# Performance work log

Measured on AMD Instinct MI355X. Metric: run time of the kernel, lower is better.

## Reference

```python
import jax, jax.numpy as jnp
import numpy as np

ALPHA = 0.2        # LeakyReLU negative slope (config['alpha'])
NEG_INF = -9e15    # mask value from the original code


def setup_inputs() -> dict:
    key = jax.random.key(0)
    k1, k2, k3, k4 = jax.random.split(key, 4)
    N, Fin, Fout = 8192, 512, 256
    inp = jax.random.normal(k1, (N, Fin), dtype=jnp.float32)
    adj = jax.random.randint(k2, (N, N), 0, 2, dtype=jnp.int32)
    # xavier_uniform with gain=1.414
    limW = 1.414 * np.sqrt(6.0 / (Fin + Fout))
    W = jax.random.uniform(k3, (Fin, Fout), dtype=jnp.float32, minval=-limW, maxval=limW)
    lima = 1.414 * np.sqrt(6.0 / (2 * Fout + 1))
    a = jax.random.uniform(k4, (2 * Fout, 1), dtype=jnp.float32, minval=-lima, maxval=lima)
    return {"input": inp, "adj": adj, "W": W, "a": a}


def reference(input, adj, W, a):
    # h: [N, F]
    h = input @ W
    Fout = W.shape[1]
    # The original builds a_input[i, j] = concat(h_i, h_j) and dots with a.
    # Equivalently: e_ij = leakyrelu(h_i . a[:F] + h_j . a[F:]), computed
    # without the O(N^2 * 2F) intermediate.
    s1 = h @ a[:Fout, 0]   # [N] contribution from node i
    s2 = h @ a[Fout:, 0]   # [N] contribution from node j
    e = s1[:, None] + s2[None, :]                     # [N, N]
    e = jnp.where(e > 0, e, ALPHA * e)                # LeakyReLU
    scores = jnp.where(adj > 0, e, NEG_INF)
    attention = jax.nn.softmax(scores, axis=1)        # row-wise softmax
    # dropout is identity in inference mode (training=False)
    h_prime = attention @ h                           # [N, F]
    return jax.nn.elu(h_prime)                        # concat=True path
```

## Files before the change

### kernel.cpp

```cpp
#include <hip/hip_runtime.h>
#include <stdint.h>
#include <stddef.h>


#define N_NODES 8192
#define FIN     512
#define FOUT    256
#define LRALPHA 0.2f
#define MI_SHIFT 16.0f

typedef float f32x4 __attribute__((ext_vector_type(4)));
typedef short s16x8 __attribute__((ext_vector_type(8)));
typedef unsigned short u16x4 __attribute__((ext_vector_type(4)));
typedef int   i32x4 __attribute__((ext_vector_type(4)));

__device__ __forceinline__ short f2bf_rne(float f) {
  uint32_t u = __builtin_bit_cast(uint32_t, f);
  u += 0x7fffu + ((u >> 16) & 1u);
  return (short)(u >> 16);
}
__device__ __forceinline__ short f2bf_fast(float f) {
  uint32_t u = __builtin_bit_cast(uint32_t, f);
  return (short)((u + 0x8000u) >> 16);
}
__device__ __forceinline__ float bf2f(short s) {
  uint32_t u = ((uint32_t)(uint16_t)s) << 16;
  return __builtin_bit_cast(float, u);
}

__global__ __launch_bounds__(256) void k_prep(const float* __restrict__ W,
                                              uint16_t* __restrict__ WThi,
                                              uint16_t* __restrict__ WTlo) {
  const int idx = blockIdx.x * 256 + threadIdx.x;
  const int n = idx >> 9;
  const int k = idx & 511;
  float v = W[k * FOUT + n];
  short h = f2bf_rne(v);
  WThi[idx] = (uint16_t)h;
  WTlo[idx] = (uint16_t)f2bf_rne(v - bf2f(h));
}

__global__ __launch_bounds__(256) void k_gemm_fused(const float* __restrict__ X,
                                                    const uint16_t* __restrict__ WThi,
                                                    const uint16_t* __restrict__ WTlo,
                                                    const float* __restrict__ a,
                                                    uint16_t* __restrict__ HTf,
                                                    float* __restrict__ s1g,
                                                    float* __restrict__ s2g) {
  __shared__ float ls1[16], ls2[16];
  __shared__ uint16_t tile[FOUT * 16];
  const int lane = threadIdx.x & 63;
  const int w    = threadIdx.x >> 6;
  const int m    = lane & 15;
  const int quad = lane >> 4;
  const int i0   = blockIdx.x * 16;
  const int colg = w * 64;

  f32x4 acc[4];
#pragma unroll
  for (int cb = 0; cb < 4; ++cb) { f32x4 z = {0.f,0.f,0.f,0.f}; acc[cb] = z; }

  for (int kt = 0; kt < FIN / 32; ++kt) {
    const int k0 = kt * 32 + quad * 8;
    const float* ap = X + (size_t)(i0 + m) * FIN + k0;
    f32x4 a0 = *(const f32x4*)ap;
    f32x4 a1 = *(const f32x4*)(ap + 4);
    s16x8 ahi, alo;
#pragma unroll
    for (int e = 0; e < 4; ++e) {
      short h0 = f2bf_rne(a0[e]); ahi[e] = h0; alo[e] = f2bf_rne(a0[e] - bf2f(h0));
      short h1 = f2bf_rne(a1[e]); ahi[4+e] = h1; alo[4+e] = f2bf_rne(a1[e] - bf2f(h1));
    }
#pragma unroll
    for (int cb = 0; cb < 4; ++cb) {
      const int n = colg + cb * 16 + m;
      s16x8 bhi = *(const s16x8*)(WThi + (size_t)n * FIN + k0);
      s16x8 blo = *(const s16x8*)(WTlo + (size_t)n * FIN + k0);
      acc[cb] = __builtin_amdgcn_mfma_f32_16x16x32_bf16(ahi, bhi, acc[cb], 0, 0, 0);
      acc[cb] = __builtin_amdgcn_mfma_f32_16x16x32_bf16(ahi, blo, acc[cb], 0, 0, 0);
      acc[cb] = __builtin_amdgcn_mfma_f32_16x16x32_bf16(alo, bhi, acc[cb], 0, 0, 0);
    }
  }

  float p1[4] = {0.f,0.f,0.f,0.f}, p2[4] = {0.f,0.f,0.f,0.f};
#pragma unroll
  for (int cb = 0; cb < 4; ++cb) {
    const int n = colg + cb * 16 + m;
    const float a1c = a[n];
    const float a2c = a[FOUT + n];
#pragma unroll
    for (int reg = 0; reg < 4; ++reg) {
      p1[reg] += acc[cb][reg] * a1c;
      p2[reg] += acc[cb][reg] * a2c;
    }
  }
#pragma unroll
  for (int off = 1; off <= 8; off <<= 1)
#pragma unroll
    for (int reg = 0; reg < 4; ++reg) {
      p1[reg] += __shfl_xor(p1[reg], off);
      p2[reg] += __shfl_xor(p2[reg], off);
    }
  if (threadIdx.x < 16) { ls1[threadIdx.x] = 0.f; ls2[threadIdx.x] = 0.f; }
  __syncthreads();
  if (m == 0) {
#pragma unroll
    for (int reg = 0; reg < 4; ++reg) {
      atomicAdd(&ls1[quad * 4 + reg], p1[reg]);
      atomicAdd(&ls2[quad * 4 + reg], p2[reg]);
    }
  }
#pragma unroll
  for (int cb = 0; cb < 4; ++cb) {
    const int col = colg + cb * 16 + m;
    u16x4 pk;
#pragma unroll
    for (int reg = 0; reg < 4; ++reg) pk[reg] = (uint16_t)f2bf_rne(acc[cb][reg]);
    *(u16x4*)(tile + col * 16 + quad * 4) = pk;
  }
  __syncthreads();
  const int t = threadIdx.x;
  if (t < 16) { s1g[i0 + t] = ls1[t]; s2g[i0 + t] = ls2[t]; }
  const int jt = i0 >> 5;
  const int qh = (i0 >> 4) & 1;
  const int c  = t >> 4;
  const int mm = t & 15;
#pragma unroll
  for (int qq = 0; qq < 2; ++qq) {
    uint4 v = *(const uint4*)(tile + (c * 16 + mm) * 16 + qq * 8);
    *(uint4*)(HTf + ((((size_t)jt * 16 + c) * 64) + (qh * 2 + qq) * 16 + mm) * 8) = v;
  }
}

__global__ __launch_bounds__(512, 8) void k_attn(const int* __restrict__ adj,
                                                 const uint16_t* __restrict__ HTf,
                                                 const float* __restrict__ s1,
                                                 const float* __restrict__ s2,
                                                 float* __restrict__ pout,
                                                 float* __restrict__ pden,
                                                 int split) {
  __shared__ uint16_t Pl[2][4096];
  __shared__ float ldsden[256];

  const int tid  = threadIdx.x;
  const int lane = tid & 63;
  const int w    = tid >> 6;
  const int m    = lane & 15;
  const int q    = lane >> 4;
  const int i0   = blockIdx.x * 32;
  const int sp   = blockIdx.y;
  const int jrange = N_NODES / split;
  const int jbeg   = sp * jrange;
  const int nphase = jrange / 128;
  const int rtp  = q >> 1;
  const int jq   = (q & 1) * 8;
  const int prow = i0 + rtp * 16 + m;

  const float s1r = s1[prow];
  float mi = s1r + MI_SHIFT; mi = mi > 0.f ? mi : LRALPHA * mi;

  f32x4 acc[2][2];
#pragma unroll
  for (int rt = 0; rt < 2; ++rt)
#pragma unroll
    for (int cb = 0; cb < 2; ++cb) { f32x4 z = {0.f,0.f,0.f,0.f}; acc[rt][cb] = z; }
  float den = 0.f;

  const int* arow = adj + (size_t)prow * N_NODES + jbeg + w * 16 + jq;
  const float* s2w = s2 + jbeg + w * 16 + jq;
  const int  pwoff = ((w * 2 + (q & 1)) * 32 + rtp * 16 + m) * 8;
  const uint16_t* hbase = HTf + ((size_t)(jbeg >> 5) * 16 + w * 2) * 64 * 8 + lane * 8;

  i32x4 A0 = *(const i32x4*)arow;
  i32x4 A1 = *(const i32x4*)(arow + 4);

#pragma unroll 1
  for (int p = 0; p < nphase; ++p) {
    const int poff = ((p + 1 < nphase) ? (p + 1) : 0) * 128;
    i32x4 nA0 = *(const i32x4*)(arow + poff);
    i32x4 nA1 = *(const i32x4*)(arow + poff + 4);
    f32x4 sv0 = *(const f32x4*)(s2w + p * 128);
    f32x4 sv1 = *(const f32x4*)(s2w + p * 128 + 4);
    s16x8 ap;
#pragma unroll
    for (int e = 0; e < 4; ++e) {
      float x = s1r + sv0[e];
      float t = x > 0.f ? x : LRALPHA * x;
      float pv = __expf(t - mi);
      pv = (A0[e] != 0) ? pv : 0.f;
      den += pv;
      ap[e] = f2bf_fast(pv);
    }
#pragma unroll
    for (int e = 0; e < 4; ++e) {
      float x = s1r + sv1[e];
      float t = x > 0.f ? x : LRALPHA * x;
      float pv = __expf(t - mi);
      pv = (A1[e] != 0) ? pv : 0.f;
      den += pv;
      ap[4 + e] = f2bf_fast(pv);
    }
    uint16_t* Pw = Pl[p & 1];
    *(s16x8*)(Pw + pwoff) = ap;
    A0 = nA0; A1 = nA1;
    __syncthreads();
    const uint16_t* hp = hbase + ((size_t)p * 4) * (16 * 64 * 8);
#pragma unroll
    for (int js = 0; js < 4; ++js) {
      s16x8 b0 = *(const s16x8*)(hp + (size_t)js * (16 * 64 * 8));
      s16x8 b1 = *(const s16x8*)(hp + (size_t)js * (16 * 64 * 8) + 64 * 8);
      const uint16_t* pc = Pw + ((js * 4 + q) * 32 + m) * 8;
      s16x8 f0 = *(const s16x8*)pc;
      s16x8 f1 = *(const s16x8*)(pc + 128);
      acc[0][0] = __builtin_amdgcn_mfma_f32_16x16x32_bf16(f0, b0, acc[0][0], 0, 0, 0);
      acc[0][1] = __builtin_amdgcn_mfma_f32_16x16x32_bf16(f0, b1, acc[0][1], 0, 0, 0);
      acc[1][0] = __builtin_amdgcn_mfma_f32_16x16x32_bf16(f1, b0, acc[1][0], 0, 0, 0);
      acc[1][1] = __builtin_amdgcn_mfma_f32_16x16x32_bf16(f1, b1, acc[1][1], 0, 0, 0);
    }
  }

  den += __shfl_xor(den, 16);
  if ((q & 1) == 0) ldsden[w * 32 + rtp * 16 + m] = den;
  __syncthreads();
  if (tid < 32) {
    float d = 0.f;
#pragma unroll
    for (int wv = 0; wv < 8; ++wv) d += ldsden[wv * 32 + tid];
    pden[(size_t)sp * N_NODES + i0 + tid] = d;
  }
  const int colg = w * 32;
#pragma unroll
  for (int rt = 0; rt < 2; ++rt)
#pragma unroll
    for (int cb = 0; cb < 2; ++cb)
#pragma unroll
      for (int reg = 0; reg < 4; ++reg) {
        const int row = i0 + rt * 16 + q * 4 + reg;
        const int col = colg + cb * 16 + m;
        pout[((size_t)sp * N_NODES + row) * FOUT + col] = acc[rt][cb][reg];
      }
}

__global__ __launch_bounds__(256) void k_reduce(const float* __restrict__ pout,
                                                const float* __restrict__ pden,
                                                float* __restrict__ out,
                                                int split) {
  const int gid = blockIdx.x * 256 + threadIdx.x;
  const int i = gid >> 6;
  const int c = (gid & 63) << 2;
  f32x4 sum = {0.f,0.f,0.f,0.f};
  float den = 0.f;
  for (int s = 0; s < split; ++s) {
    sum += *(const f32x4*)(pout + ((size_t)s * N_NODES + i) * FOUT + c);
    den += pden[(size_t)s * N_NODES + i];
  }
  const float inv = 1.0f / den;
  f32x4 r;
#pragma unroll
  for (int e = 0; e < 4; ++e) {
    float v = sum[e] * inv;
    r[e] = v > 0.f ? v : (__expf(v) - 1.0f);
  }
  *(f32x4*)(out + (size_t)i * FOUT + c) = r;
}

extern "C" void kernel_launch(void* const* d_in, const int* in_sizes, int n_in,
                              void* d_out, int out_size, void* d_ws, size_t ws_size,
                              hipStream_t stream) {
  const float* X   = (const float*)d_in[0];
  const int*   adj = (const int*)d_in[1];
  const float* W   = (const float*)d_in[2];
  const float* a   = (const float*)d_in[3];
  float* out = (float*)d_out;

  char* ws = (char*)d_ws;
  uint16_t* HTf  = (uint16_t*)ws;
  uint16_t* WThi = (uint16_t*)(ws + (4u << 20));
  uint16_t* WTlo = WThi + (size_t)FOUT * FIN;
  float*    s1   = (float*)(ws + (4u << 20) + (512u << 10));
  float*    s2   = s1 + N_NODES;
  float*    pden = s2 + N_NODES;
  const size_t pout_off = (size_t)5u << 20;
  const size_t slab = (size_t)N_NODES * FOUT * sizeof(float);

  int split;
  if      (ws_size >= pout_off + 4 * slab) split = 4;
  else if (ws_size >= pout_off + 2 * slab) split = 2;
  else                                     split = 1;
  float* pout = (split == 1) ? out : (float*)(ws + pout_off);

  k_prep<<<dim3(512), dim3(256), 0, stream>>>(W, WThi, WTlo);
  k_gemm_fused<<<dim3(N_NODES / 16), dim3(256), 0, stream>>>(X, WThi, WTlo, a, HTf, s1, s2);
  k_attn<<<dim3(N_NODES / 32, split), dim3(512), 0, stream>>>(adj, HTf, s1, s2, pout, pden, split);
  k_reduce<<<dim3(N_NODES * FOUT / 4 / 256), dim3(256), 0, stream>>>(pout, pden, out, split);
}
```

Baseline: 474.0 us.

## Pack adjacency into bitmask and enlarge attention tile to 64 rows

Adds a pre-pass kernel that compresses the int32 adjacency matrix into a per-row bitmask using wave ballots. The attention kernel then reads that compact mask instead of the full int matrix. The attention tile grows to 64 rows by 256 columns per block, with s2 staged in LDS and B-operand loads split around the barrier to overlap with the exp work. The goal is less adjacency traffic in the attention loop and more reuse of H per block. The cost is an extra full pass over adj, more registers, and lower occupancy (launch bounds 4 instead of 8).

```diff
diff --git a/kernel.cpp b/kernel.cpp
--- a/kernel.cpp
+++ b/kernel.cpp
@@ -13,6 +13,7 @@
 typedef short s16x8 __attribute__((ext_vector_type(8)));
 typedef unsigned short u16x4 __attribute__((ext_vector_type(4)));
 typedef int   i32x4 __attribute__((ext_vector_type(4)));
+typedef unsigned long long u64;
 
 __device__ __forceinline__ short f2bf_rne(float f) {
   uint32_t u = __builtin_bit_cast(uint32_t, f);
@@ -26,6 +27,38 @@
 __device__ __forceinline__ float bf2f(short s) {
   uint32_t u = ((uint32_t)(uint16_t)s) << 16;
   return __builtin_bit_cast(float, u);
+}
+
+__global__ __launch_bounds__(256) void k_mask(const int* __restrict__ adj,
+                                              uint32_t* __restrict__ M3) {
+  const int row = blockIdx.x;
+  const int w   = threadIdx.x >> 6;
+  const int L   = threadIdx.x & 63;
+  const int c   = L >> 2;
+  const int J   = L & 3;
+  const int ch  = c >> 3;
+  const int cb  = (c & 7) * 8;
+  const int* base = adj + (size_t)row * N_NODES + w * 2048;
+  uint32_t accum = 0;
+#pragma unroll
+  for (int gg = 0; gg < 8; ++gg) {
+    int v0 = base[gg * 256 + L];
+    int v1 = base[gg * 256 + 64 + L];
+    int v2 = base[gg * 256 + 128 + L];
+    int v3 = base[gg * 256 + 192 + L];
+    u64 b0 = __ballot(v0 != 0);
+    u64 b1 = __ballot(v1 != 0);
+    u64 b2 = __ballot(v2 != 0);
+    u64 b3 = __ballot(v3 != 0);
+#pragma unroll
+    for (int th = 0; th < 2; ++th) {
+      u64 bsel = ch ? (th ? b3 : b1) : (th ? b2 : b0);
+      int slot = 2 * gg + th - J * 4;
+      uint32_t byte = (uint32_t)(bsel >> cb) & 0xffu;
+      accum |= (slot >= 0 && slot < 4) ? (byte << (8 * (slot & 3))) : 0u;
+    }
+  }
+  M3[(size_t)row * 256 + c * 16 + w * 4 + J] = accum;
 }
 
 __global__ __launch_bounds__(256) void k_prep(const float* __restrict__ W,
@@ -132,111 +165,137 @@
   }
 }
 
-__global__ __launch_bounds__(512, 8) void k_attn(const int* __restrict__ adj,
+__global__ __launch_bounds__(512, 4) void k_attn(const uint32_t* __restrict__ M3,
                                                  const uint16_t* __restrict__ HTf,
                                                  const float* __restrict__ s1,
                                                  const float* __restrict__ s2,
                                                  float* __restrict__ pout,
                                                  float* __restrict__ pden,
                                                  int split) {
-  __shared__ uint16_t Pl[2][4096];
-  __shared__ float ldsden[256];
+  __shared__ uint16_t PL[2][8192];
+  __shared__ float lss2[2048];
+  __shared__ float ldsden[512];
 
   const int tid  = threadIdx.x;
   const int lane = tid & 63;
   const int w    = tid >> 6;
   const int m    = lane & 15;
   const int q    = lane >> 4;
-  const int i0   = blockIdx.x * 32;
+  const int rl   = lane & 31;
+  const int cpr  = w * 2 + (lane >> 5);
+  const int cg   = w & 3, rg = w >> 2;
+  const int i0   = blockIdx.x * 64;
   const int sp   = blockIdx.y;
   const int jrange = N_NODES / split;
   const int jbeg   = sp * jrange;
-  const int nphase = jrange / 128;
-  const int rtp  = q >> 1;
-  const int jq   = (q & 1) * 8;
-  const int prow = i0 + rtp * 16 + m;
-
-  const float s1r = s1[prow];
-  float mi = s1r + MI_SHIFT; mi = mi > 0.f ? mi : LRALPHA * mi;
-
-  f32x4 acc[2][2];
+  const int npb    = jrange / 2048;
+
+  const float s1r0 = s1[i0 + rl];
+  const float s1r1 = s1[i0 + 32 + rl];
+  float mi0 = fmaxf(s1r0 + MI_SHIFT, LRALPHA * (s1r0 + MI_SHIFT));
+  float mi1 = fmaxf(s1r1 + MI_SHIFT, LRALPHA * (s1r1 + MI_SHIFT));
+
+  f32x4 acc[2][4];
 #pragma unroll
   for (int rt = 0; rt < 2; ++rt)
 #pragma unroll
-    for (int cb = 0; cb < 2; ++cb) { f32x4 z = {0.f,0.f,0.f,0.f}; acc[rt][cb] = z; }
-  float den = 0.f;
-
-  const int* arow = adj + (size_t)prow * N_NODES + jbeg + w * 16 + jq;
-  const float* s2w = s2 + jbeg + w * 16 + jq;
-  const int  pwoff = ((w * 2 + (q & 1)) * 32 + rtp * 16 + m) * 8;
-  const uint16_t* hbase = HTf + ((size_t)(jbeg >> 5) * 16 + w * 2) * 64 * 8 + lane * 8;
-
-  i32x4 A0 = *(const i32x4*)arow;
-  i32x4 A1 = *(const i32x4*)(arow + 4);
+    for (int cb = 0; cb < 4; ++cb) { f32x4 z = {0.f,0.f,0.f,0.f}; acc[rt][cb] = z; }
+  float den0 = 0.f, den1 = 0.f;
+
+  const uint8_t* mrow0 = (const uint8_t*)M3 + ((size_t)(i0 + rl) << 10) + cpr * 64 + (jbeg >> 7);
+  const uint8_t* mrow1 = mrow0 + (32u << 10);
+  const int pwoff = (cpr * 64 + rl) * 8;
+  const uint16_t* hB = HTf + ((size_t)(jbeg >> 5) * 16 + cg * 4) * 512 + lane * 8;
 
 #pragma unroll 1
-  for (int p = 0; p < nphase; ++p) {
-    const int poff = ((p + 1 < nphase) ? (p + 1) : 0) * 128;
-    i32x4 nA0 = *(const i32x4*)(arow + poff);
-    i32x4 nA1 = *(const i32x4*)(arow + poff + 4);
-    f32x4 sv0 = *(const f32x4*)(s2w + p * 128);
-    f32x4 sv1 = *(const f32x4*)(s2w + p * 128 + 4);
-    s16x8 ap;
-#pragma unroll
-    for (int e = 0; e < 4; ++e) {
-      float x = s1r + sv0[e];
-      float t = x > 0.f ? x : LRALPHA * x;
-      float pv = __expf(t - mi);
-      pv = (A0[e] != 0) ? pv : 0.f;
-      den += pv;
-      ap[e] = f2bf_fast(pv);
-    }
-#pragma unroll
-    for (int e = 0; e < 4; ++e) {
-      float x = s1r + sv1[e];
-      float t = x > 0.f ? x : LRALPHA * x;
-      float pv = __expf(t - mi);
-      pv = (A1[e] != 0) ? pv : 0.f;
-      den += pv;
-      ap[4 + e] = f2bf_fast(pv);
-    }
-    uint16_t* Pw = Pl[p & 1];
-    *(s16x8*)(Pw + pwoff) = ap;
-    A0 = nA0; A1 = nA1;
+  for (int pb = 0; pb < npb; ++pb) {
+    f32x4 sstage = *(const f32x4*)(s2 + jbeg + pb * 2048 + tid * 4);
+    uint4 mk0 = *(const uint4*)(mrow0 + pb * 16);
+    uint4 mk1 = *(const uint4*)(mrow1 + pb * 16);
+    const u64 m0lo = mk0.x | ((u64)mk0.y << 32), m0hi = mk0.z | ((u64)mk0.w << 32);
+    const u64 m1lo = mk1.x | ((u64)mk1.y << 32), m1hi = mk1.z | ((u64)mk1.w << 32);
+    *(f32x4*)(lss2 + tid * 4) = sstage;
     __syncthreads();
-    const uint16_t* hp = hbase + ((size_t)p * 4) * (16 * 64 * 8);
-#pragma unroll
-    for (int js = 0; js < 4; ++js) {
-      s16x8 b0 = *(const s16x8*)(hp + (size_t)js * (16 * 64 * 8));
-      s16x8 b1 = *(const s16x8*)(hp + (size_t)js * (16 * 64 * 8) + 64 * 8);
-      const uint16_t* pc = Pw + ((js * 4 + q) * 32 + m) * 8;
-      s16x8 f0 = *(const s16x8*)pc;
-      s16x8 f1 = *(const s16x8*)(pc + 128);
-      acc[0][0] = __builtin_amdgcn_mfma_f32_16x16x32_bf16(f0, b0, acc[0][0], 0, 0, 0);
-      acc[0][1] = __builtin_amdgcn_mfma_f32_16x16x32_bf16(f0, b1, acc[0][1], 0, 0, 0);
-      acc[1][0] = __builtin_amdgcn_mfma_f32_16x16x32_bf16(f1, b0, acc[1][0], 0, 0, 0);
-      acc[1][1] = __builtin_amdgcn_mfma_f32_16x16x32_bf16(f1, b1, acc[1][1], 0, 0, 0);
-    }
-  }
-
-  den += __shfl_xor(den, 16);
-  if ((q & 1) == 0) ldsden[w * 32 + rtp * 16 + m] = den;
+
+#pragma unroll 1
+    for (int pp = 0; pp < 16; ++pp) {
+      s16x8 B[4][4];
+      const uint16_t* hp = hB + (size_t)((pb * 16 + pp) * 4) * (16 * 512);
+#pragma unroll
+      for (int js = 0; js < 2; ++js)
+#pragma unroll
+        for (int cb = 0; cb < 4; ++cb)
+          B[js][cb] = *(const s16x8*)(hp + (size_t)js * (16 * 512) + cb * 512);
+      const u64 sel0 = (pp & 8) ? m0hi : m0lo;
+      const u64 sel1 = (pp & 8) ? m1hi : m1lo;
+      const uint32_t by0 = (uint32_t)(sel0 >> ((pp & 7) * 8)) & 0xffu;
+      const uint32_t by1 = (uint32_t)(sel1 >> ((pp & 7) * 8)) & 0xffu;
+      f32x4 sA = *(const f32x4*)(lss2 + pp * 128 + cpr * 8);
+      f32x4 sB = *(const f32x4*)(lss2 + pp * 128 + cpr * 8 + 4);
+      s16x8 P0, P1;
+#pragma unroll
+      for (int e = 0; e < 4; ++e) {
+        float x0 = s1r0 + sA[e];
+        float p0 = __expf(fmaxf(x0, LRALPHA * x0) - mi0);
+        p0 = ((by0 >> e) & 1u) ? p0 : 0.f;
+        den0 += p0; P0[e] = f2bf_fast(p0);
+        float x1 = s1r0 + sB[e];
+        float p1v = __expf(fmaxf(x1, LRALPHA * x1) - mi0);
+        p1v = ((by0 >> (e + 4)) & 1u) ? p1v : 0.f;
+        den0 += p1v; P0[4 + e] = f2bf_fast(p1v);
+        float x2 = s1r1 + sA[e];
+        float p2v = __expf(fmaxf(x2, LRALPHA * x2) - mi1);
+        p2v = ((by1 >> e) & 1u) ? p2v : 0.f;
+        den1 += p2v; P1[e] = f2bf_fast(p2v);
+        float x3 = s1r1 + sB[e];
+        float p3v = __expf(fmaxf(x3, LRALPHA * x3) - mi1);
+        p3v = ((by1 >> (e + 4)) & 1u) ? p3v : 0.f;
+        den1 += p3v; P1[4 + e] = f2bf_fast(p3v);
+      }
+      uint16_t* Pw = PL[pp & 1];
+      *(s16x8*)(Pw + pwoff) = P0;
+      *(s16x8*)(Pw + pwoff + 32 * 8) = P1;
+#pragma unroll
+      for (int js = 2; js < 4; ++js)
+#pragma unroll
+        for (int cb = 0; cb < 4; ++cb)
+          B[js][cb] = *(const s16x8*)(hp + (size_t)js * (16 * 512) + cb * 512);
+      __syncthreads();
+#pragma unroll
+      for (int js = 0; js < 4; ++js) {
+        const uint16_t* pc = Pw + ((js * 4 + q) * 64 + rg * 32 + m) * 8;
+        s16x8 f0 = *(const s16x8*)pc;
+        s16x8 f1 = *(const s16x8*)(pc + 16 * 8);
+#pragma unroll
+        for (int cb = 0; cb < 4; ++cb) {
+          acc[0][cb] = __builtin_amdgcn_mfma_f32_16x16x32_bf16(f0, B[js][cb], acc[0][cb], 0, 0, 0);
+          acc[1][cb] = __builtin_amdgcn_mfma_f32_16x16x32_bf16(f1, B[js][cb], acc[1][cb], 0, 0, 0);
+        }
+      }
+    }
+  }
+
+  den0 += __shfl_xor(den0, 32);
+  den1 += __shfl_xor(den1, 32);
+  if (lane < 32) {
+    ldsden[w * 64 + rl] = den0;
+    ldsden[w * 64 + 32 + rl] = den1;
+  }
   __syncthreads();
-  if (tid < 32) {
+  if (tid < 64) {
     float d = 0.f;
 #pragma unroll
-    for (int wv = 0; wv < 8; ++wv) d += ldsden[wv * 32 + tid];
+    for (int wv = 0; wv < 8; ++wv) d += ldsden[wv * 64 + tid];
     pden[(size_t)sp * N_NODES + i0 + tid] = d;
   }
-  const int colg = w * 32;
 #pragma unroll
   for (int rt = 0; rt < 2; ++rt)
 #pragma unroll
-    for (int cb = 0; cb < 2; ++cb)
+    for (int cb = 0; cb < 4; ++cb)
 #pragma unroll
       for (int reg = 0; reg < 4; ++reg) {
-        const int row = i0 + rt * 16 + q * 4 + reg;
-        const int col = colg + cb * 16 + m;
+        const int row = i0 + rg * 32 + rt * 16 + q * 4 + reg;
+        const int col = cg * 64 + cb * 16 + m;
         pout[((size_t)sp * N_NODES + row) * FOUT + col] = acc[rt][cb][reg];
       }
 }
@@ -276,11 +335,12 @@
   char* ws = (char*)d_ws;
   uint16_t* HTf  = (uint16_t*)ws;
   uint16_t* WThi = (uint16_t*)(ws + (4u << 20));
-  uint16_t* WTlo = WThi + (size_t)FOUT * FIN;
-  float*    s1   = (float*)(ws + (4u << 20) + (512u << 10));
+  uint16_t* WTlo = (uint16_t*)(ws + (4u << 20) + 262144);
+  float*    s1   = (float*)(ws + (4u << 20) + 524288);
   float*    s2   = s1 + N_NODES;
   float*    pden = s2 + N_NODES;
-  const size_t pout_off = (size_t)5u << 20;
+  uint32_t* M3   = (uint32_t*)(ws + (6u << 20));
+  const size_t pout_off = (size_t)16u << 20;
   const size_t slab = (size_t)N_NODES * FOUT * sizeof(float);
 
   int split;
@@ -290,7 +350,8 @@
   float* pout = (split == 1) ? out : (float*)(ws + pout_off);
 
   k_prep<<<dim3(512), dim3(256), 0, stream>>>(W, WThi, WTlo);
+  k_mask<<<dim3(N_NODES), dim3(256), 0, stream>>>(adj, M3);
   k_gemm_fused<<<dim3(N_NODES / 16), dim3(256), 0, stream>>>(X, WThi, WTlo, a, HTf, s1, s2);
-  k_attn<<<dim3(N_NODES / 32, split), dim3(512), 0, stream>>>(adj, HTf, s1, s2, pout, pden, split);
+  k_attn<<<dim3(N_NODES / 64, split), dim3(512), 0, stream>>>(M3, HTf, s1, s2, pout, pden, split);
   k_reduce<<<dim3(N_NODES * FOUT / 4 / 256), dim3(256), 0, stream>>>(pout, pden, out, split);
 }
```

Result: slower. 546.8 us (+15.4%).

## Pack adjacency into bitmasks in GEMM kernel and enlarge attention row tile

Applied to the files above, without the earlier changes.

Adds extra blocks to the feature GEMM kernel that read the int32 adjacency matrix once and pack it into 64-bit ballot bitmasks. The attention kernel then reads these compact masks instead of the full int32 adjacency. The attention kernel's row tile grows from 32 to 128 rows, with 4x4 MFMA accumulators per wave, so each H tile loaded is reused across more rows. s2 is staged in LDS, and split-K can now go up to 8. The cost is higher register pressure from the larger accumulators, lower declared occupancy, more partial-output traffic in the reduce step, and a larger workspace footprint.

```diff
diff --git a/kernel.cpp b/kernel.cpp
--- a/kernel.cpp
+++ b/kernel.cpp
@@ -13,6 +13,7 @@
 typedef short s16x8 __attribute__((ext_vector_type(8)));
 typedef unsigned short u16x4 __attribute__((ext_vector_type(4)));
 typedef int   i32x4 __attribute__((ext_vector_type(4)));
+typedef unsigned long long u64;
 
 __device__ __forceinline__ short f2bf_rne(float f) {
   uint32_t u = __builtin_bit_cast(uint32_t, f);
@@ -40,17 +41,47 @@
   WTlo[idx] = (uint16_t)f2bf_rne(v - bf2f(h));
 }
 
-__global__ __launch_bounds__(256) void k_gemm_fused(const float* __restrict__ X,
-                                                    const uint16_t* __restrict__ WThi,
-                                                    const uint16_t* __restrict__ WTlo,
-                                                    const float* __restrict__ a,
-                                                    uint16_t* __restrict__ HTf,
-                                                    float* __restrict__ s1g,
-                                                    float* __restrict__ s2g) {
+__global__ __launch_bounds__(256, 4) void k_pre(const float* __restrict__ X,
+                                                const uint16_t* __restrict__ WThi,
+                                                const uint16_t* __restrict__ WTlo,
+                                                const float* __restrict__ a,
+                                                const int* __restrict__ adj,
+                                                uint16_t* __restrict__ HTf,
+                                                float* __restrict__ s1g,
+                                                float* __restrict__ s2g,
+                                                u64* __restrict__ M3) {
   __shared__ float ls1[16], ls2[16];
   __shared__ uint16_t tile[FOUT * 16];
   const int lane = threadIdx.x & 63;
   const int w    = threadIdx.x >> 6;
+
+  if (blockIdx.x >= 512) {
+    const int bxm  = blockIdx.x - 512;
+    const int iblk = bxm >> 5;
+    const int jc   = bxm & 31;
+    const int L    = lane;
+    const int* base = adj + (size_t)(iblk * 128 + w * 32) * N_NODES + jc * 256 + L;
+    u64 keep0 = 0, keep1 = 0, keep2 = 0, keep3 = 0;
+#pragma unroll
+    for (int it = 0; it < 32; ++it) {
+      const int* rp = base + (size_t)it * N_NODES;
+      int v0 = rp[0], v1 = rp[64], v2 = rp[128], v3 = rp[192];
+      u64 b0 = __ballot(v0 != 0);
+      u64 b1 = __ballot(v1 != 0);
+      u64 b2 = __ballot(v2 != 0);
+      u64 b3 = __ballot(v3 != 0);
+      if (L == it) { keep0 = b0; keep1 = b1; keep2 = b2; keep3 = b3; }
+    }
+    if (L < 32) {
+      const size_t mb = (size_t)iblk * 128 * 128 + (w * 32 + L);
+      M3[mb + (size_t)(jc * 4 + 0) * 128] = keep0;
+      M3[mb + (size_t)(jc * 4 + 1) * 128] = keep1;
+      M3[mb + (size_t)(jc * 4 + 2) * 128] = keep2;
+      M3[mb + (size_t)(jc * 4 + 3) * 128] = keep3;
+    }
+    return;
+  }
+
   const int m    = lane & 15;
   const int quad = lane >> 4;
   const int i0   = blockIdx.x * 16;
@@ -132,111 +163,106 @@
   }
 }
 
-__global__ __launch_bounds__(512, 8) void k_attn(const int* __restrict__ adj,
+__global__ __launch_bounds__(512, 4) void k_attn(const u64* __restrict__ M3,
                                                  const uint16_t* __restrict__ HTf,
                                                  const float* __restrict__ s1,
                                                  const float* __restrict__ s2,
                                                  float* __restrict__ pout,
                                                  float* __restrict__ pden,
                                                  int split) {
-  __shared__ uint16_t Pl[2][4096];
-  __shared__ float ldsden[256];
+  __shared__ uint16_t PL[2][4096];
+  __shared__ float lss2[1024];
+  __shared__ float ldsden[512];
 
   const int tid  = threadIdx.x;
   const int lane = tid & 63;
   const int w    = tid >> 6;
   const int m    = lane & 15;
   const int q    = lane >> 4;
-  const int i0   = blockIdx.x * 32;
+  const int rg   = w >> 2, cg = w & 3;
+  const int r    = tid & 127;
+  const int cpr  = tid >> 7;
+  const int i0   = blockIdx.x * 128;
   const int sp   = blockIdx.y;
   const int jrange = N_NODES / split;
   const int jbeg   = sp * jrange;
-  const int nphase = jrange / 128;
-  const int rtp  = q >> 1;
-  const int jq   = (q & 1) * 8;
-  const int prow = i0 + rtp * 16 + m;
-
-  const float s1r = s1[prow];
-  float mi = s1r + MI_SHIFT; mi = mi > 0.f ? mi : LRALPHA * mi;
-
-  f32x4 acc[2][2];
-#pragma unroll
-  for (int rt = 0; rt < 2; ++rt)
-#pragma unroll
-    for (int cb = 0; cb < 2; ++cb) { f32x4 z = {0.f,0.f,0.f,0.f}; acc[rt][cb] = z; }
+  const int nphase = jrange / 32;
+
+  const float s1r = s1[i0 + r];
+  float mi = fmaxf(s1r + MI_SHIFT, LRALPHA * (s1r + MI_SHIFT));
+
+  f32x4 acc[4][4];
+#pragma unroll
+  for (int rt = 0; rt < 4; ++rt)
+#pragma unroll
+    for (int cb = 0; cb < 4; ++cb) { f32x4 z = {0.f,0.f,0.f,0.f}; acc[rt][cb] = z; }
   float den = 0.f;
 
-  const int* arow = adj + (size_t)prow * N_NODES + jbeg + w * 16 + jq;
-  const float* s2w = s2 + jbeg + w * 16 + jq;
-  const int  pwoff = ((w * 2 + (q & 1)) * 32 + rtp * 16 + m) * 8;
-  const uint16_t* hbase = HTf + ((size_t)(jbeg >> 5) * 16 + w * 2) * 64 * 8 + lane * 8;
-
-  i32x4 A0 = *(const i32x4*)arow;
-  i32x4 A1 = *(const i32x4*)(arow + 4);
+  const u64* mrow = M3 + ((size_t)blockIdx.x * 128 + (jbeg >> 6)) * 128 + r;
+  u64 mcur = mrow[0];
 
 #pragma unroll 1
-  for (int p = 0; p < nphase; ++p) {
-    const int poff = ((p + 1 < nphase) ? (p + 1) : 0) * 128;
-    i32x4 nA0 = *(const i32x4*)(arow + poff);
-    i32x4 nA1 = *(const i32x4*)(arow + poff + 4);
-    f32x4 sv0 = *(const f32x4*)(s2w + p * 128);
-    f32x4 sv1 = *(const f32x4*)(s2w + p * 128 + 4);
-    s16x8 ap;
-#pragma unroll
-    for (int e = 0; e < 4; ++e) {
-      float x = s1r + sv0[e];
-      float t = x > 0.f ? x : LRALPHA * x;
-      float pv = __expf(t - mi);
-      pv = (A0[e] != 0) ? pv : 0.f;
-      den += pv;
-      ap[e] = f2bf_fast(pv);
-    }
-#pragma unroll
-    for (int e = 0; e < 4; ++e) {
-      float x = s1r + sv1[e];
-      float t = x > 0.f ? x : LRALPHA * x;
-      float pv = __expf(t - mi);
-      pv = (A1[e] != 0) ? pv : 0.f;
-      den += pv;
-      ap[4 + e] = f2bf_fast(pv);
-    }
-    uint16_t* Pw = Pl[p & 1];
-    *(s16x8*)(Pw + pwoff) = ap;
-    A0 = nA0; A1 = nA1;
-    __syncthreads();
-    const uint16_t* hp = hbase + ((size_t)p * 4) * (16 * 64 * 8);
-#pragma unroll
-    for (int js = 0; js < 4; ++js) {
-      s16x8 b0 = *(const s16x8*)(hp + (size_t)js * (16 * 64 * 8));
-      s16x8 b1 = *(const s16x8*)(hp + (size_t)js * (16 * 64 * 8) + 64 * 8);
-      const uint16_t* pc = Pw + ((js * 4 + q) * 32 + m) * 8;
-      s16x8 f0 = *(const s16x8*)pc;
-      s16x8 f1 = *(const s16x8*)(pc + 128);
-      acc[0][0] = __builtin_amdgcn_mfma_f32_16x16x32_bf16(f0, b0, acc[0][0], 0, 0, 0);
-      acc[0][1] = __builtin_amdgcn_mfma_f32_16x16x32_bf16(f0, b1, acc[0][1], 0, 0, 0);
-      acc[1][0] = __builtin_amdgcn_mfma_f32_16x16x32_bf16(f1, b0, acc[1][0], 0, 0, 0);
-      acc[1][1] = __builtin_amdgcn_mfma_f32_16x16x32_bf16(f1, b1, acc[1][1], 0, 0, 0);
-    }
-  }
-
-  den += __shfl_xor(den, 16);
-  if ((q & 1) == 0) ldsden[w * 32 + rtp * 16 + m] = den;
+  for (int ph = 0; ph < nphase; ph += 2) {
+    if ((ph & 31) == 0) {
+      __syncthreads();
+      if (tid < 256) *(f32x4*)(lss2 + tid * 4) =
+        *(const f32x4*)(s2 + jbeg + (ph >> 5) * 1024 + tid * 4);
+      __syncthreads();
+    }
+    u64 mnx = (ph + 2 < nphase) ? mrow[((ph >> 1) + 1) * 128] : 0;
+#pragma unroll
+    for (int po = 0; po < 2; ++po) {
+      const int p = ph + po;
+      const int pl = p & 31;
+      f32x4 sA = *(const f32x4*)(lss2 + pl * 32 + cpr * 8);
+      f32x4 sB = *(const f32x4*)(lss2 + pl * 32 + cpr * 8 + 4);
+      const uint32_t by = (uint32_t)(mcur >> ((po * 4 + cpr) * 8)) & 0xffu;
+      s16x8 P0;
+#pragma unroll
+      for (int e = 0; e < 4; ++e) {
+        float x0 = s1r + sA[e];
+        float pv0 = __expf(fmaxf(x0, LRALPHA * x0) - mi);
+        pv0 = ((by >> e) & 1u) ? pv0 : 0.f;
+        den += pv0; P0[e] = f2bf_fast(pv0);
+        float x1 = s1r + sB[e];
+        float pv1 = __expf(fmaxf(x1, LRALPHA * x1) - mi);
+        pv1 = ((by >> (e + 4)) & 1u) ? pv1 : 0.f;
+        den += pv1; P0[4 + e] = f2bf_fast(pv1);
+      }
+      *(s16x8*)(PL[p & 1] + (cpr * 128 + r) * 8) = P0;
+      __syncthreads();
+      const uint16_t* hB = HTf + ((size_t)((jbeg >> 5) + p) * 16 + cg * 4) * 512 + lane * 8;
+      s16x8 Bv[4];
+#pragma unroll
+      for (int cb = 0; cb < 4; ++cb)
+        Bv[cb] = *(const s16x8*)(hB + cb * 512);
+      s16x8 F[4];
+#pragma unroll
+      for (int rt = 0; rt < 4; ++rt)
+        F[rt] = *(const s16x8*)(PL[p & 1] + (q * 128 + rg * 64 + rt * 16 + m) * 8);
+#pragma unroll
+      for (int rt = 0; rt < 4; ++rt)
+#pragma unroll
+        for (int cb = 0; cb < 4; ++cb)
+          acc[rt][cb] = __builtin_amdgcn_mfma_f32_16x16x32_bf16(F[rt], Bv[cb], acc[rt][cb], 0, 0, 0);
+    }
+    mcur = mnx;
+  }
+
+  ldsden[cpr * 128 + r] = den;
   __syncthreads();
-  if (tid < 32) {
-    float d = 0.f;
-#pragma unroll
-    for (int wv = 0; wv < 8; ++wv) d += ldsden[wv * 32 + tid];
+  if (tid < 128) {
+    float d = ldsden[tid] + ldsden[128 + tid] + ldsden[256 + tid] + ldsden[384 + tid];
     pden[(size_t)sp * N_NODES + i0 + tid] = d;
   }
-  const int colg = w * 32;
-#pragma unroll
-  for (int rt = 0; rt < 2; ++rt)
-#pragma unroll
-    for (int cb = 0; cb < 2; ++cb)
+#pragma unroll
+  for (int rt = 0; rt < 4; ++rt)
+#pragma unroll
+    for (int cb = 0; cb < 4; ++cb)
 #pragma unroll
       for (int reg = 0; reg < 4; ++reg) {
-        const int row = i0 + rt * 16 + q * 4 + reg;
-        const int col = colg + cb * 16 + m;
+        const int row = i0 + rg * 64 + rt * 16 + q * 4 + reg;
+        const int col = cg * 64 + cb * 16 + m;
         pout[((size_t)sp * N_NODES + row) * FOUT + col] = acc[rt][cb][reg];
       }
 }
@@ -276,21 +302,23 @@
   char* ws = (char*)d_ws;
   uint16_t* HTf  = (uint16_t*)ws;
   uint16_t* WThi = (uint16_t*)(ws + (4u << 20));
-  uint16_t* WTlo = WThi + (size_t)FOUT * FIN;
-  float*    s1   = (float*)(ws + (4u << 20) + (512u << 10));
+  uint16_t* WTlo = (uint16_t*)(ws + (4u << 20) + 262144);
+  float*    s1   = (float*)(ws + (4u << 20) + 524288);
   float*    s2   = s1 + N_NODES;
   float*    pden = s2 + N_NODES;
-  const size_t pout_off = (size_t)5u << 20;
+  u64*      M3   = (u64*)(ws + (6u << 20));
+  const size_t pout_off = (size_t)16u << 20;
   const size_t slab = (size_t)N_NODES * FOUT * sizeof(float);
 
   int split;
-  if      (ws_size >= pout_off + 4 * slab) split = 4;
+  if      (ws_size >= pout_off + 8 * slab) split = 8;
+  else if (ws_size >= pout_off + 4 * slab) split = 4;
   else if (ws_size >= pout_off + 2 * slab) split = 2;
   else                                     split = 1;
   float* pout = (split == 1) ? out : (float*)(ws + pout_off);
 
   k_prep<<<dim3(512), dim3(256), 0, stream>>>(W, WThi, WTlo);
-  k_gemm_fused<<<dim3(N_NODES / 16), dim3(256), 0, stream>>>(X, WThi, WTlo, a, HTf, s1, s2);
-  k_attn<<<dim3(N_NODES / 32, split), dim3(512), 0, stream>>>(adj, HTf, s1, s2, pout, pden, split);
+  k_pre<<<dim3(2560), dim3(256), 0, stream>>>(X, WThi, WTlo, a, adj, HTf, s1, s2, M3);
+  k_attn<<<dim3(N_NODES / 128, split), dim3(512), 0, stream>>>(M3, HTf, s1, s2, pout, pden, split);
   k_reduce<<<dim3(N_NODES * FOUT / 4 / 256), dim3(256), 0, stream>>>(pout, pden, out, split);
 }
```

Measured after the change: 473.0 us. Within noise of the previous version (-0.2%).
